# Kernel optimization log

Hardware: AMD Instinct MI355X
Metric: run time of the kernel (lower is better)

## Reference

```python
import jax, jax.numpy as jnp
import numpy as np

NUM_ITER = 20
EPS = 1e-12


def sinkhorn_knopp(m):
    # m: [B, C, C] logits -> doubly stochastic matrix
    m = jnp.nan_to_num(m, nan=0.0, posinf=0.0, neginf=0.0)
    m = m - jnp.max(m, axis=-1, keepdims=True)
    K = jnp.exp(m)

    def body(_, K):
        K = K / (jnp.sum(K, axis=-1, keepdims=True) + EPS)
        K = K / (jnp.sum(K, axis=-2, keepdims=True) + EPS)
        return K

    return jax.lax.fori_loop(0, NUM_ITER, body, K)


def setup_inputs() -> dict:
    key = jax.random.key(0)
    k_x, k_w1, k_w2 = jax.random.split(key, 3)
    B, C, H, W = 32, 256, 64, 64
    R = 64  # reduced_dim = C // 4
    x = jax.random.normal(k_x, (B, C, H, W), dtype=jnp.float32)
    # 1x1 convs on [B,C,1,1] are linear layers; store weights as [out, in]
    w1 = jax.random.normal(k_w1, (R, C), dtype=jnp.float32) * (1.0 / np.sqrt(C))
    b1 = jnp.zeros((R,), dtype=jnp.float32)
    w2 = jax.random.normal(k_w2, (C * C, R), dtype=jnp.float32) * (1.0 / np.sqrt(R))
    b2 = jnp.zeros((C * C,), dtype=jnp.float32)
    scale = jnp.full((1,), 0.01, dtype=jnp.float32)
    return {"x": x, "w1": w1, "b1": b1, "w2": w2, "b2": b2, "scale": scale}


def reference(x, w1, b1, w2, b2, scale):
    B, C, H, W = x.shape
    pooled = jnp.mean(x, axis=(2, 3))              # [B, C] (AdaptiveAvgPool2d(1))
    h = jax.nn.silu(pooled @ w1.T + b1)            # [B, R]
    weights = (h @ w2.T + b2).reshape(B, C, C)     # [B, C, C]
    M = sinkhorn_knopp(weights)                    # [B, C, C]
    x_flat = x.reshape(B, C, H * W)                # [B, C, HW]
    x_mixed = jnp.einsum('bij,bjs->bis', M, x_flat).reshape(B, C, H, W)
    return x + scale * x_mixed
```

## Files before the change

kernel.cpp:

```cpp
#include <hip/hip_runtime.h>
#include <hip/hip_bf16.h>
#include <math.h>

#define SK_EPS 1e-12f

typedef __attribute__((ext_vector_type(8))) short short8;
typedef __attribute__((ext_vector_type(4))) float f32x4;

__device__ __forceinline__ unsigned short f2bf(float f) {
  union { float f; unsigned int u; } c; c.f = f;
  unsigned int u = c.u + 0x7FFFu + ((c.u >> 16) & 1u);
  return (unsigned short)(u >> 16);
}
__device__ __forceinline__ float bflo(unsigned int u) {
  union { unsigned int i; float f; } c; c.i = u << 16; return c.f;
}
__device__ __forceinline__ float bfhi(unsigned int u) {
  union { unsigned int i; float f; } c; c.i = u & 0xffff0000u; return c.f;
}

__global__ __launch_bounds__(256) void pool_k(const float* __restrict__ x,
                                              float* __restrict__ pooled) {
  const int row = blockIdx.x;
  const float4* xr = reinterpret_cast<const float4*>(x + (size_t)row * 4096);
  const int t = threadIdx.x;
  float s = 0.0f;
#pragma unroll
  for (int k = 0; k < 4; ++k) {
    float4 v = xr[t + k * 256];
    s += v.x + v.y + v.z + v.w;
  }
#pragma unroll
  for (int m = 1; m < 64; m <<= 1) s += __shfl_xor(s, m);
  __shared__ float wsum[4];
  if ((t & 63) == 0) wsum[t >> 6] = s;
  __syncthreads();
  if (t == 0) pooled[row] = (wsum[0] + wsum[1] + wsum[2] + wsum[3]) * (1.0f / 4096.0f);
}

__global__ __launch_bounds__(64) void h_k(const float* __restrict__ pooled,
                                          const float* __restrict__ w1,
                                          const float* __restrict__ b1,
                                          float* __restrict__ h) {
  const int b = blockIdx.x;
  const int r = threadIdx.x;
  const float4* p4 = reinterpret_cast<const float4*>(pooled + b * 256);
  const float4* w4 = reinterpret_cast<const float4*>(w1 + r * 256);
  float acc = b1[r];
#pragma unroll 8
  for (int k = 0; k < 64; ++k) {
    float4 a = p4[k], w = w4[k];
    acc += a.x * w.x + a.y * w.y + a.z * w.z + a.w * w.w;
  }
  float sig = 1.0f / (1.0f + __expf(-acc));
  h[b * 64 + r] = acc * sig;
}

__global__ __launch_bounds__(256) void wgen_k(const float* __restrict__ h,
                                              const float* __restrict__ w2,
                                              const float* __restrict__ b2,
                                              float* __restrict__ wout) {
  __shared__ float hs[32][64];
  const int t = threadIdx.x;
  for (int i = t; i < 2048; i += 256) hs[i >> 6][i & 63] = h[i];
  __syncthreads();
  const int n = blockIdx.x * 256 + t;
  float4 wr[16];
  const float4* w4 = reinterpret_cast<const float4*>(w2 + (size_t)n * 64);
#pragma unroll
  for (int k = 0; k < 16; ++k) wr[k] = w4[k];
  const float bias = b2[n];
  for (int b = 0; b < 32; ++b) {
    const float4* hb = reinterpret_cast<const float4*>(hs[b]);
    float acc = bias;
#pragma unroll
    for (int k = 0; k < 16; ++k) {
      float4 hv = hb[k];
      acc += wr[k].x * hv.x + wr[k].y * hv.y + wr[k].z * hv.z + wr[k].w * hv.w;
    }
    wout[(size_t)b * 65536 + n] = acc;
  }
}

__global__ __launch_bounds__(1024) void sink_k(const float* __restrict__ Wsrc,
                                               unsigned short* __restrict__ Mout) {
  const int b = blockIdx.x;
  const int t = threadIdx.x;
  const int ti = t >> 5, tj = t & 31;
  const int R0 = ti * 8, C0 = tj * 8;
  const float* W = Wsrc + (size_t)b * 65536;

  __shared__ __align__(16) unsigned short Ksh[65536];
  __shared__ float part[16][256];
  __shared__ float colsum[256];

  float rmax[8];
#pragma unroll
  for (int ii = 0; ii < 8; ++ii) {
    float4 v0 = *reinterpret_cast<const float4*>(W + (size_t)(R0 + ii) * 256 + C0);
    float4 v1 = *reinterpret_cast<const float4*>(W + (size_t)(R0 + ii) * 256 + C0 + 4);
    float a[8] = {v0.x, v0.y, v0.z, v0.w, v1.x, v1.y, v1.z, v1.w};
    float m = -3.4e38f;
#pragma unroll
    for (int jj = 0; jj < 8; ++jj) {
      float v = isfinite(a[jj]) ? a[jj] : 0.0f;
      m = fmaxf(m, v);
    }
    rmax[ii] = m;
  }
#pragma unroll
  for (int msk = 1; msk < 32; msk <<= 1)
#pragma unroll
    for (int ii = 0; ii < 8; ++ii) rmax[ii] = fmaxf(rmax[ii], __shfl_xor(rmax[ii], msk));

#pragma unroll
  for (int ii = 0; ii < 8; ++ii) {
    float4 v0 = *reinterpret_cast<const float4*>(W + (size_t)(R0 + ii) * 256 + C0);
    float4 v1 = *reinterpret_cast<const float4*>(W + (size_t)(R0 + ii) * 256 + C0 + 4);
    float a[8] = {v0.x, v0.y, v0.z, v0.w, v1.x, v1.y, v1.z, v1.w};
    unsigned int pk[4];
#pragma unroll
    for (int hh = 0; hh < 4; ++hh) {
      float x0 = isfinite(a[2 * hh]) ? a[2 * hh] : 0.0f;
      float x1 = isfinite(a[2 * hh + 1]) ? a[2 * hh + 1] : 0.0f;
      float e0 = __expf(x0 - rmax[ii]);
      float e1 = __expf(x1 - rmax[ii]);
      pk[hh] = (unsigned int)f2bf(e0) | ((unsigned int)f2bf(e1) << 16);
    }
    uint4 u = {pk[0], pk[1], pk[2], pk[3]};
    *reinterpret_cast<uint4*>(Ksh + (size_t)(R0 + ii) * 256 + C0) = u;
  }
  __syncthreads();

  float ru[8], cv[8];
#pragma unroll
  for (int k = 0; k < 8; ++k) { ru[k] = 1.0f; cv[k] = 1.0f; }
  const int w = t >> 6;

  for (int it = 0; it < 20; ++it) {
    float p[8];
#pragma unroll
    for (int ii = 0; ii < 8; ++ii) {
      uint4 kv = *reinterpret_cast<const uint4*>(Ksh + (size_t)(R0 + ii) * 256 + C0);
      float s = bflo(kv.x) * cv[0] + bfhi(kv.x) * cv[1]
              + bflo(kv.y) * cv[2] + bfhi(kv.y) * cv[3]
              + bflo(kv.z) * cv[4] + bfhi(kv.z) * cv[5]
              + bflo(kv.w) * cv[6] + bfhi(kv.w) * cv[7];
      p[ii] = s;
    }
#pragma unroll
    for (int msk = 1; msk < 32; msk <<= 1)
#pragma unroll
      for (int ii = 0; ii < 8; ++ii) p[ii] += __shfl_xor(p[ii], msk);
#pragma unroll
    for (int ii = 0; ii < 8; ++ii)
      ru[ii] = ru[ii] * __builtin_amdgcn_rcpf(ru[ii] * p[ii] + SK_EPS);

    float q[8] = {0, 0, 0, 0, 0, 0, 0, 0};
#pragma unroll
    for (int ii = 0; ii < 8; ++ii) {
      uint4 kv = *reinterpret_cast<const uint4*>(Ksh + (size_t)(R0 + ii) * 256 + C0);
      float r = ru[ii];
      q[0] += bflo(kv.x) * r; q[1] += bfhi(kv.x) * r;
      q[2] += bflo(kv.y) * r; q[3] += bfhi(kv.y) * r;
      q[4] += bflo(kv.z) * r; q[5] += bfhi(kv.z) * r;
      q[6] += bflo(kv.w) * r; q[7] += bfhi(kv.w) * r;
    }
#pragma unroll
    for (int jj = 0; jj < 8; ++jj) q[jj] += __shfl_xor(q[jj], 32);
    if ((t & 32) == 0) {
      float4 q0 = {q[0], q[1], q[2], q[3]};
      float4 q1 = {q[4], q[5], q[6], q[7]};
      *reinterpret_cast<float4*>(&part[w][tj * 8]) = q0;
      *reinterpret_cast<float4*>(&part[w][tj * 8 + 4]) = q1;
    }
    __syncthreads();
    if (t < 256) {
      float s = 0.0f;
#pragma unroll
      for (int ww = 0; ww < 16; ++ww) s += part[ww][t];
      colsum[t] = s;
    }
    __syncthreads();
    float4 c0 = *reinterpret_cast<float4*>(&colsum[C0]);
    float4 c1 = *reinterpret_cast<float4*>(&colsum[C0 + 4]);
    float cs[8] = {c0.x, c0.y, c0.z, c0.w, c1.x, c1.y, c1.z, c1.w};
#pragma unroll
    for (int jj = 0; jj < 8; ++jj)
      cv[jj] = cv[jj] * __builtin_amdgcn_rcpf(cv[jj] * cs[jj] + SK_EPS);
  }

  unsigned short* Mo = Mout + (size_t)b * 65536;
#pragma unroll
  for (int ii = 0; ii < 8; ++ii) {
    uint4 kv = *reinterpret_cast<const uint4*>(Ksh + (size_t)(R0 + ii) * 256 + C0);
    float r = ru[ii];
    float f[8] = {bflo(kv.x) * r * cv[0], bfhi(kv.x) * r * cv[1],
                  bflo(kv.y) * r * cv[2], bfhi(kv.y) * r * cv[3],
                  bflo(kv.z) * r * cv[4], bfhi(kv.z) * r * cv[5],
                  bflo(kv.w) * r * cv[6], bfhi(kv.w) * r * cv[7]};
    unsigned int pk[4];
#pragma unroll
    for (int hh = 0; hh < 4; ++hh)
      pk[hh] = (unsigned int)f2bf(f[2 * hh]) | ((unsigned int)f2bf(f[2 * hh + 1]) << 16);
    uint4 u = {pk[0], pk[1], pk[2], pk[3]};
    *reinterpret_cast<uint4*>(Mo + (size_t)(R0 + ii) * 256 + C0) = u;
  }
}

__global__ __launch_bounds__(512) void mix_k(const float* __restrict__ x,
                                             const unsigned short* __restrict__ M,
                                             const float* __restrict__ scale,
                                             float* __restrict__ out) {
  const int sb = blockIdx.x;
  const int b = blockIdx.y;
  const int s0 = sb * 32;
  const float* xb = x + (size_t)b * 1048576;
  float* ob = out + (size_t)b * 1048576;
  const unsigned short* Mb = M + (size_t)b * 65536;

  __shared__ __align__(16) unsigned short XT[8192];
  char* XTb = reinterpret_cast<char*>(XT);
  const int t = threadIdx.x;

#pragma unroll
  for (int it = 0; it < 4; ++it) {
    int fidx = t + it * 512;
    int j = fidx >> 3, sq = fidx & 7;
    float4 v = *reinterpret_cast<const float4*>(xb + (size_t)j * 4096 + s0 + sq * 4);
    float vv[4] = {v.x, v.y, v.z, v.w};
#pragma unroll
    for (int c = 0; c < 4; ++c) {
      int sl = sq * 4 + c;
      int byteoff = (sl * 512 + j * 2) ^ ((sl & 7) << 4);
      *reinterpret_cast<unsigned short*>(XTb + byteoff) = f2bf(vv[c]);
    }
  }
  __syncthreads();

  const int lane = t & 63, wave = t >> 6;
  const int wrow = wave >> 1;
  const int wcol = wave & 1;
  const int l15 = lane & 15, l4 = lane >> 4;

  f32x4 acc[4] = {{0.f, 0.f, 0.f, 0.f}, {0.f, 0.f, 0.f, 0.f},
                  {0.f, 0.f, 0.f, 0.f}, {0.f, 0.f, 0.f, 0.f}};

  const int sl = wcol * 16 + l15;
#pragma unroll
  for (int k0 = 0; k0 < 256; k0 += 32) {
    int bo = (sl * 512 + (k0 + l4 * 8) * 2) ^ ((sl & 7) << 4);
    short8 bfrag = *reinterpret_cast<const short8*>(XTb + bo);
#pragma unroll
    for (int mf = 0; mf < 4; ++mf) {
      int i = wrow * 64 + mf * 16 + l15;
      short8 afrag = *reinterpret_cast<const short8*>(Mb + (size_t)i * 256 + k0 + l4 * 8);
      acc[mf] = __builtin_amdgcn_mfma_f32_16x16x32_bf16(afrag, bfrag, acc[mf], 0, 0, 0);
    }
  }

  const float sc = scale[0];
#pragma unroll
  for (int mf = 0; mf < 4; ++mf) {
#pragma unroll
    for (int r = 0; r < 4; ++r) {
      int i = wrow * 64 + mf * 16 + l4 * 4 + r;
      int s = s0 + wcol * 16 + l15;
      size_t off = (size_t)i * 4096 + s;
      ob[off] = xb[off] + sc * acc[mf][r];
    }
  }
}

extern "C" void kernel_launch(void* const* d_in, const int* in_sizes, int n_in,
                              void* d_out, int out_size, void* d_ws, size_t ws_size,
                              hipStream_t stream) {
  const float* x = (const float*)d_in[0];
  const float* w1 = (const float*)d_in[1];
  const float* b1 = (const float*)d_in[2];
  const float* w2 = (const float*)d_in[3];
  const float* b2 = (const float*)d_in[4];
  const float* scale = (const float*)d_in[5];
  float* out = (float*)d_out;

  char* ws = (char*)d_ws;
  float* pooled = (float*)(ws);
  float* hbuf = (float*)(ws + 32768);
  float* wbuf = (float*)(ws + 40960);
  unsigned short* Mbuf = (unsigned short*)(ws + 40960 + 8388608);

  pool_k<<<8192, 256, 0, stream>>>(x, pooled);
  h_k<<<32, 64, 0, stream>>>(pooled, w1, b1, hbuf);
  wgen_k<<<256, 256, 0, stream>>>(hbuf, w2, b2, wbuf);
  sink_k<<<32, 1024, 0, stream>>>(wbuf, Mbuf);
  mix_k<<<dim3(128, 32), 512, 0, stream>>>(x, Mbuf, scale, out);
}
```

Measured before the change: 460.8 us.

## Store mixing matrix in MFMA fragment order and widen mix tile to 64 columns

The Sinkhorn kernel now writes M in a pre-swizzled MFMA A-fragment layout, so mix_k loads each fragment as one contiguous coalesced 16-byte read per lane. mix_k processes 64 spatial columns per block instead of 32, reusing each M fragment across two N-fragments, halving the grid and the total M reads. The X tile is transposed into fragment order through lane shuffles and vectorized LDS writes. It also adds a waves_per_eu hint. The costs are more registers and LDS per block and fewer blocks.

Measured after the change: 427.1 us. -7.3%, faster.

```diff
diff --git a/kernel.cpp b/kernel.cpp
--- a/kernel.cpp
+++ b/kernel.cpp
@@ -17,6 +17,12 @@
 }
 __device__ __forceinline__ float bfhi(unsigned int u) {
   union { unsigned int i; float f; } c; c.i = u & 0xffff0000u; return c.f;
+}
+
+__device__ __forceinline__ int mfrag_us(int i, int c) {
+  int wrow = i >> 6, mf = (i >> 4) & 3, l15 = i & 15;
+  int k0idx = c >> 2, l4 = c & 3;
+  return ((((wrow * 8 + k0idx) * 4 + mf) * 64) + l4 * 16 + l15) * 8;
 }
 
 __global__ __launch_bounds__(256) void pool_k(const float* __restrict__ x,
@@ -204,72 +210,90 @@
     for (int hh = 0; hh < 4; ++hh)
       pk[hh] = (unsigned int)f2bf(f[2 * hh]) | ((unsigned int)f2bf(f[2 * hh + 1]) << 16);
     uint4 u = {pk[0], pk[1], pk[2], pk[3]};
-    *reinterpret_cast<uint4*>(Mo + (size_t)(R0 + ii) * 256 + C0) = u;
-  }
-}
-
-__global__ __launch_bounds__(512) void mix_k(const float* __restrict__ x,
-                                             const unsigned short* __restrict__ M,
-                                             const float* __restrict__ scale,
-                                             float* __restrict__ out) {
+    *reinterpret_cast<uint4*>(Mo + mfrag_us(R0 + ii, tj)) = u;
+  }
+}
+
+__global__ __launch_bounds__(512) __attribute__((amdgpu_waves_per_eu(2)))
+void mix_k(const float* __restrict__ x,
+           const unsigned short* __restrict__ Mf,
+           const float* __restrict__ scale,
+           float* __restrict__ out) {
   const int sb = blockIdx.x;
   const int b = blockIdx.y;
-  const int s0 = sb * 32;
+  const int s0 = sb * 64;
   const float* xb = x + (size_t)b * 1048576;
   float* ob = out + (size_t)b * 1048576;
-  const unsigned short* Mb = M + (size_t)b * 65536;
-
-  __shared__ __align__(16) unsigned short XT[8192];
-  char* XTb = reinterpret_cast<char*>(XT);
-  const int t = threadIdx.x;
-
-#pragma unroll
-  for (int it = 0; it < 4; ++it) {
-    int fidx = t + it * 512;
-    int j = fidx >> 3, sq = fidx & 7;
-    float4 v = *reinterpret_cast<const float4*>(xb + (size_t)j * 4096 + s0 + sq * 4);
-    float vv[4] = {v.x, v.y, v.z, v.w};
-#pragma unroll
-    for (int c = 0; c < 4; ++c) {
-      int sl = sq * 4 + c;
-      int byteoff = (sl * 512 + j * 2) ^ ((sl & 7) << 4);
-      *reinterpret_cast<unsigned short*>(XTb + byteoff) = f2bf(vv[c]);
-    }
+  const unsigned short* Mb = Mf + (size_t)b * 65536;
+
+  __shared__ __align__(16) unsigned short XT[16384];
+  const int t = threadIdx.x, lane = t & 63, w = t >> 6;
+  const int jq = lane & 3, sq = lane >> 2;
+
+#pragma unroll
+  for (int it = 0; it < 8; ++it) {
+    int j0 = (it * 8 + w) * 4;
+    float4 v = *reinterpret_cast<const float4*>(xb + (size_t)(j0 + jq) * 4096 + s0 + sq * 4);
+    float a0 = v.x, a1 = v.y, a2 = v.z, a3 = v.w;
+    float s0_ = __shfl_xor(a0, 1), s1_ = __shfl_xor(a1, 1);
+    float s2_ = __shfl_xor(a2, 1), s3_ = __shfl_xor(a3, 1);
+    float w0 = (jq & 1) ? s1_ : a0;
+    float w1 = (jq & 1) ? a1 : s0_;
+    float w2 = (jq & 1) ? s3_ : a2;
+    float w3 = (jq & 1) ? a3 : s2_;
+    float t0 = __shfl_xor(w0, 2), t1 = __shfl_xor(w1, 2);
+    float t2 = __shfl_xor(w2, 2), t3 = __shfl_xor(w3, 2);
+    float W0 = (jq & 2) ? t2 : w0;
+    float W1 = (jq & 2) ? t3 : w1;
+    float W2 = (jq & 2) ? t0 : w2;
+    float W3 = (jq & 2) ? t1 : w3;
+    unsigned int u0 = (unsigned int)f2bf(W0) | ((unsigned int)f2bf(W1) << 16);
+    unsigned int u1 = (unsigned int)f2bf(W2) | ((unsigned int)f2bf(W3) << 16);
+    uint2 uu = {u0, u1};
+    int usidx = ((j0 >> 3) * 64 + lane) * 8 + (j0 & 4);
+    *reinterpret_cast<uint2*>(XT + usidx) = uu;
   }
   __syncthreads();
 
-  const int lane = t & 63, wave = t >> 6;
-  const int wrow = wave >> 1;
-  const int wcol = wave & 1;
+  const int wrow = w >> 1;
+  const int wcol = w & 1;
   const int l15 = lane & 15, l4 = lane >> 4;
 
-  f32x4 acc[4] = {{0.f, 0.f, 0.f, 0.f}, {0.f, 0.f, 0.f, 0.f},
-                  {0.f, 0.f, 0.f, 0.f}, {0.f, 0.f, 0.f, 0.f}};
-
-  const int sl = wcol * 16 + l15;
-#pragma unroll
-  for (int k0 = 0; k0 < 256; k0 += 32) {
-    int bo = (sl * 512 + (k0 + l4 * 8) * 2) ^ ((sl & 7) << 4);
-    short8 bfrag = *reinterpret_cast<const short8*>(XTb + bo);
+  f32x4 acc[4][2];
+#pragma unroll
+  for (int mf = 0; mf < 4; ++mf)
+#pragma unroll
+    for (int nf = 0; nf < 2; ++nf) acc[mf][nf] = {0.f, 0.f, 0.f, 0.f};
+
+#pragma unroll
+  for (int k0 = 0; k0 < 8; ++k0) {
+    short8 bfrag[2];
+#pragma unroll
+    for (int nf = 0; nf < 2; ++nf) {
+      int us = ((k0 * 4 + l4) * 64 + wcol * 32 + nf * 16 + l15) * 8;
+      bfrag[nf] = *reinterpret_cast<const short8*>(XT + us);
+    }
 #pragma unroll
     for (int mf = 0; mf < 4; ++mf) {
-      int i = wrow * 64 + mf * 16 + l15;
-      short8 afrag = *reinterpret_cast<const short8*>(Mb + (size_t)i * 256 + k0 + l4 * 8);
-      acc[mf] = __builtin_amdgcn_mfma_f32_16x16x32_bf16(afrag, bfrag, acc[mf], 0, 0, 0);
+      const short8 afrag = *reinterpret_cast<const short8*>(
+          Mb + ((((wrow * 8 + k0) * 4 + mf) * 64) + lane) * 8);
+      acc[mf][0] = __builtin_amdgcn_mfma_f32_16x16x32_bf16(afrag, bfrag[0], acc[mf][0], 0, 0, 0);
+      acc[mf][1] = __builtin_amdgcn_mfma_f32_16x16x32_bf16(afrag, bfrag[1], acc[mf][1], 0, 0, 0);
     }
   }
 
   const float sc = scale[0];
 #pragma unroll
-  for (int mf = 0; mf < 4; ++mf) {
-#pragma unroll
-    for (int r = 0; r < 4; ++r) {
-      int i = wrow * 64 + mf * 16 + l4 * 4 + r;
-      int s = s0 + wcol * 16 + l15;
-      size_t off = (size_t)i * 4096 + s;
-      ob[off] = xb[off] + sc * acc[mf][r];
-    }
-  }
+  for (int mf = 0; mf < 4; ++mf)
+#pragma unroll
+    for (int nf = 0; nf < 2; ++nf)
+#pragma unroll
+      for (int r = 0; r < 4; ++r) {
+        int i = wrow * 64 + mf * 16 + l4 * 4 + r;
+        int s = s0 + wcol * 32 + nf * 16 + l15;
+        size_t off = (size_t)i * 4096 + s;
+        ob[off] = xb[off] + sc * acc[mf][nf][r];
+      }
 }
 
 extern "C" void kernel_launch(void* const* d_in, const int* in_sizes, int n_in,
@@ -293,5 +317,5 @@
   h_k<<<32, 64, 0, stream>>>(pooled, w1, b1, hbuf);
   wgen_k<<<256, 256, 0, stream>>>(hbuf, w2, b2, wbuf);
   sink_k<<<32, 1024, 0, stream>>>(wbuf, Mbuf);
-  mix_k<<<dim3(128, 32), 512, 0, stream>>>(x, Mbuf, scale, out);
-}
+  mix_k<<<dim3(64, 32), 512, 0, stream>>>(x, Mbuf, scale, out);
+}
```
